# Kernel tuning notes

Measured on AMD Instinct MI355X. Metric: run time of the kernel, lower is better.

## Reference

```python
import jax, jax.numpy as jnp
import numpy as np

V, E, U, B, S = 32000, 512, 1024, 16, 128
BN_EPS = 1e-3  # keras BatchNormalization default


def setup_inputs() -> dict:
    key = jax.random.key(0)
    ks = jax.random.split(key, 12)
    w = 0.05  # small init keeps the relu-activated LSTM recurrence stable
    return {
        "inputs": jax.random.randint(ks[0], (B, S), 0, V),
        "enc_hidden": jax.random.normal(ks[1], (B, U), jnp.float32) * 0.1,
        "enc_cell": jax.random.normal(ks[2], (B, U), jnp.float32) * 0.1,
        "emb": jax.random.normal(ks[3], (V, E), jnp.float32) * w,
        "Wx": jax.random.normal(ks[4], (E, 4 * U), jnp.float32) * w,
        "Wh": jax.random.normal(ks[5], (U, 4 * U), jnp.float32) * w,
        "b": jnp.zeros((4 * U,), jnp.float32),
        "gamma": jnp.ones((U,), jnp.float32),
        "beta": jnp.zeros((U,), jnp.float32),
        "mov_mean": jnp.zeros((U,), jnp.float32),
        "mov_var": jnp.ones((U,), jnp.float32),
        "W1": jax.random.normal(ks[6], (U, U), jnp.float32) * w,
        "b1": jnp.zeros((U,), jnp.float32),
        "W2": jax.random.normal(ks[7], (U, V), jnp.float32) * w,
        "b2": jnp.zeros((V,), jnp.float32),
    }


def _lstm_relu(xg, mask, h0, c0, Wh):
    # xg: [S,B,4U] precomputed input gates; mask: [S,B] (mask_zero semantics)
    def step(carry, inp):
        h, c = carry
        g, m = inp
        z = g + h @ Wh  # [B,4U]
        i, f, cc, o = jnp.split(z, 4, axis=-1)  # keras gate order i,f,c,o
        i = jax.nn.sigmoid(i)
        f = jax.nn.sigmoid(f)
        o = jax.nn.sigmoid(o)
        cc = jax.nn.relu(cc)  # activation='relu' on candidate
        c_new = f * c + i * cc
        h_new = o * jax.nn.relu(c_new)  # activation='relu' on output
        m = m[:, None]
        h_new = jnp.where(m, h_new, h)  # masked step: carry state/output
        c_new = jnp.where(m, c_new, c)
        return (h_new, c_new), h_new

    (_, _), hs = jax.lax.scan(step, (h0, c0), (xg, mask))
    return hs  # [S,B,U]


def reference(inputs, enc_hidden, enc_cell, emb, Wx, Wh, b, gamma, beta,
              mov_mean, mov_var, W1, b1, W2, b2):
    x = emb[inputs]                       # [B,S,E]
    mask = (inputs != 0)                  # mask_zero=True
    xg = jnp.einsum("bse,eg->bsg", x, Wx) + b   # [B,S,4U]
    hs = _lstm_relu(xg.transpose(1, 0, 2), mask.T, enc_hidden, enc_cell, Wh)
    h = hs.transpose(1, 0, 2)             # [B,S,U]
    # BatchNorm (inference: moving statistics), Dropout is identity at inference
    hbn = (h - mov_mean) * jax.lax.rsqrt(mov_var + BN_EPS) * gamma + beta
    d1 = jax.nn.relu(hbn @ W1 + b1)       # [B,S,U]
    logits = d1 @ W2 + b2                 # [B,S,V]
    return jax.nn.softmax(logits, axis=-1)
```

## Files before the change

### kernel.cpp

```cpp
#include <hip/hip_runtime.h>
#include <hip/hip_bf16.h>
#include <stdint.h>

typedef unsigned short u16;
typedef unsigned int u32;
typedef unsigned long long u64;
typedef __attribute__((ext_vector_type(4))) float f32x4;
typedef __attribute__((ext_vector_type(8))) short s16x8;

#define AT_LD(p)    __hip_atomic_load((p), __ATOMIC_RELAXED, __HIP_MEMORY_SCOPE_AGENT)
#define AT_ST(p, v) __hip_atomic_store((p), (v), __ATOMIC_RELAXED, __HIP_MEMORY_SCOPE_AGENT)


static __device__ __forceinline__ u16 f2bf(float f) {
  union { float f; unsigned u; } v; v.f = f;
  unsigned r = v.u + 0x7FFFu + ((v.u >> 16) & 1u);
  return (u16)(r >> 16);
}

static __device__ __forceinline__ void gload_lds16(const void* g, void* l) {
  __builtin_amdgcn_global_load_lds(
      (const __attribute__((address_space(1))) unsigned int*)(uintptr_t)g,
      (__attribute__((address_space(3))) unsigned int*)(uintptr_t)l,
      16, 0, 0);
}

static __device__ __forceinline__ int swzB(int B) {
  int pos = (B >> 4) & 127;
  int row = (B >> 11) & 15;
  int slot = (pos ^ row ^ (pos >> 3)) & 7;
  int npos = (pos & 0x78) | slot;
  return (B & ~0x7F0) | (npos << 4);
}


__global__ void embed_kernel(const int* __restrict__ inputs,
                             const float* __restrict__ emb,
                             u16* __restrict__ xbf) {
  int i = blockIdx.x * 256 + threadIdx.x;
  int row = i >> 6;
  int e0 = (i & 63) << 3;
  int tok = inputs[row];
  const float* src = emb + (size_t)tok * 512 + e0;
  s16x8 o;
#pragma unroll
  for (int j = 0; j < 8; ++j) o[j] = (short)f2bf(src[j]);
  *(s16x8*)(xbf + (size_t)row * 512 + e0) = o;
}

__global__ void mask_kernel(const int* __restrict__ inputs, u64* __restrict__ mb) {
  int t = threadIdx.x;
  if (t < 32) {
    int b = t >> 1, h = t & 1;
    u64 m = 0;
    for (int j = 0; j < 64; ++j)
      m |= (u64)(inputs[b * 128 + h * 64 + j] != 0) << j;
    mb[t] = m;
  }
}

__global__ void transpose_bf16(const float* __restrict__ W, u16* __restrict__ Wt,
                               int K, int N) {
  __shared__ float t[32][33];
  int ntn = N >> 5;
  int tn = blockIdx.x % ntn, tk = blockIdx.x / ntn;
  int n0 = tn << 5, k0 = tk << 5;
  int tx = threadIdx.x & 31, ty = threadIdx.x >> 5;
#pragma unroll
  for (int j = 0; j < 4; ++j) {
    int k = ty * 4 + j;
    t[k][tx] = W[(size_t)(k0 + k) * N + n0 + tx];
  }
  __syncthreads();
#pragma unroll
  for (int j = 0; j < 4; ++j) {
    int n = ty * 4 + j;
    Wt[(size_t)(n0 + n) * K + k0 + tx] = f2bf(t[tx][n]);
  }
}

template <int MODE>
__global__ __launch_bounds__(256)
void gemm_bf16(const u16* __restrict__ A, const u16* __restrict__ Bt,
               const float* __restrict__ bias, void* __restrict__ Cptr,
               float* __restrict__ rowsum, int M, int N, int K) {
  (void)M;
  __shared__ u16 sA[128 * 32];
  __shared__ u16 sB[128 * 32];
  const int nbn = N >> 7;
  const int nwg = gridDim.x;
  int bid = blockIdx.x;
  int q = nwg >> 3;
  int swz = (bid & 7) * q + (bid >> 3);
  int bm = swz / nbn, bn = swz % nbn;
  const int brow = bm << 7, bcol = bn << 7;

  const int tid = threadIdx.x;
  const int lane = tid & 63;
  const int wv = tid >> 6;
  const int wr = (wv >> 1) * 64, wc = (wv & 1) * 64;
  const int ln = lane & 15, kh = lane >> 4;

  const int srow = tid >> 2;
  const int kch = (tid & 3) << 3;

  f32x4 acc[4][4] = {};

  const int nk = K >> 5;
  const u16* Abase = A + (size_t)(brow + srow) * K + kch;
  const u16* Bbase = Bt + (size_t)(bcol + srow) * K + kch;
  const size_t rstride = (size_t)64 * K;
  u16* lA = sA + srow * 32 + kch;
  u16* lB = sB + srow * 32 + kch;

  for (int kt = 0; kt < nk; ++kt) {
    const int k0 = kt << 5;
    gload_lds16(Abase + k0, lA);
    gload_lds16(Abase + rstride + k0, lA + 64 * 32);
    gload_lds16(Bbase + k0, lB);
    gload_lds16(Bbase + rstride + k0, lB + 64 * 32);
    __syncthreads();
    s16x8 aF[4], bF[4];
#pragma unroll
    for (int m = 0; m < 4; ++m)
      aF[m] = *(const s16x8*)(sA + (wr + m * 16 + ln) * 32 + kh * 8);
#pragma unroll
    for (int n = 0; n < 4; ++n)
      bF[n] = *(const s16x8*)(sB + (wc + n * 16 + ln) * 32 + kh * 8);
#pragma unroll
    for (int m = 0; m < 4; ++m)
#pragma unroll
      for (int n = 0; n < 4; ++n)
        acc[m][n] = __builtin_amdgcn_mfma_f32_16x16x32_bf16(aF[m], bF[n], acc[m][n], 0, 0, 0);
    __syncthreads();
  }

  const int browq = brow + wr;
  const int bcolq = bcol + wc;

  if (MODE == 1) {
    u16* O = (u16*)Cptr;
#pragma unroll
    for (int n = 0; n < 4; ++n) {
      int gcol = bcolq + n * 16 + ln;
      float bv = bias[gcol];
#pragma unroll
      for (int m = 0; m < 4; ++m)
#pragma unroll
        for (int r = 0; r < 4; ++r) {
          int grow = browq + m * 16 + kh * 4 + r;
          float v = fmaxf(acc[m][n][r] + bv, 0.f);
          O[(size_t)grow * N + gcol] = f2bf(v);
        }
    }
  } else {
    float* O = (float*)Cptr;
    float rs[4][4] = {};
#pragma unroll
    for (int n = 0; n < 4; ++n) {
      int gcol = bcolq + n * 16 + ln;
      float bv = bias[gcol];
#pragma unroll
      for (int m = 0; m < 4; ++m)
#pragma unroll
        for (int r = 0; r < 4; ++r) {
          int grow = browq + m * 16 + kh * 4 + r;
          float v = acc[m][n][r] + bv;
          if (MODE == 2) { v = __expf(v); rs[m][r] += v; }
          O[(size_t)grow * N + gcol] = v;
        }
    }
    if (MODE == 2) {
#pragma unroll
      for (int m = 0; m < 4; ++m)
#pragma unroll
        for (int r = 0; r < 4; ++r) {
          float v = rs[m][r];
          v += __shfl_xor(v, 1);
          v += __shfl_xor(v, 2);
          v += __shfl_xor(v, 4);
          v += __shfl_xor(v, 8);
          if (ln == 0) atomicAdd(&rowsum[browq + m * 16 + kh * 4 + r], v);
        }
    }
  }
}

__global__ __launch_bounds__(256, 1)
void lstm_kernel(const float* __restrict__ xg,
                 const u16* __restrict__ Wht,
                 const u64* __restrict__ maskb,
                 const float* __restrict__ ench, const float* __restrict__ encc,
                 const float* __restrict__ gamma, const float* __restrict__ beta,
                 const float* __restrict__ mmean, const float* __restrict__ mvar,
                 u32* __restrict__ hbuf32,
                 u16* __restrict__ hbn,
                 u32* __restrict__ cnt) {
  __shared__ char hA[32 * 1024];

  const int wg = blockIdx.x;
  const int u0 = wg << 4;
  const int tid = threadIdx.x;
  const int lane = tid & 63;
  const int wv = tid >> 6;
  const int ln = lane & 15, kh = lane >> 4;

  const int g = ln & 3;
  const int ul = ln >> 2;
  const int unit = u0 + wv * 4 + ul;

  s16x8 bW[32];
  {
    const u16* wrow = Wht + (size_t)(g * 1024 + unit) * 1024 + kh * 8;
#pragma unroll
    for (int kt = 0; kt < 32; ++kt)
      bW[kt] = *(const s16x8*)(wrow + kt * 32);
  }

  float cellR[4], holdR[4];
  u64 mA[4], mB[4];
  const float bn_s = gamma[unit] * rsqrtf(mvar[unit] + 1e-3f);
  const float bn_b = beta[unit] - mmean[unit] * bn_s;
#pragma unroll
  for (int r = 0; r < 4; ++r) {
    int batch = kh * 4 + r;
    cellR[r] = encc[batch * 1024 + unit];
    holdR[r] = ench[batch * 1024 + unit];
    mA[r] = maskb[batch * 2];
    mB[r] = maskb[batch * 2 + 1];
  }

#pragma unroll
  for (int r = 0; r < 4; ++r) {
    u32 w = (u32)f2bf(holdR[r]);
    u32 pw = (u32)__shfl_xor((int)w, 4);
    if ((ln & 7) == 0) {
      int batch = kh * 4 + r;
      int B = batch * 2048 + unit * 2;
      AT_ST((u32*)((char*)hbuf32 + B), (w & 0xFFFFu) | (pw << 16));
    }
  }
  asm volatile("s_waitcnt vmcnt(0)" ::: "memory");
  __syncthreads();
  if (tid == 0) {
    (void)__hip_atomic_fetch_add(cnt, 1, __ATOMIC_RELAXED, __HIP_MEMORY_SCOPE_AGENT);
    int c = 0;
    while (AT_LD((const u32*)cnt) < 64u) { if (++c > (1 << 20)) break; }
  }
  __syncthreads();

  const size_t bstride = (size_t)128 * 4096;
  const float* xbase = xg + (size_t)(kh * 4) * bstride + g * 1024 + unit;
  float xgr[4];
#pragma unroll
  for (int r = 0; r < 4; ++r) xgr[r] = xbase[r * bstride];

  for (int s = 0; s < 128; ++s) {
    const u64* src = (const u64*)((const char*)hbuf32 + (s & 1) * 32768) + tid;
    u64 st[16];
#pragma unroll
    for (int k = 0; k < 16; ++k) st[k] = AT_LD(src + k * 256);
#pragma unroll
    for (int k = 0; k < 16; ++k)
      *(u64*)(hA + swzB(k * 2048 + tid * 8)) = st[k];
    __syncthreads();

    f32x4 acc0 = {0.f, 0.f, 0.f, 0.f};
    f32x4 acc1 = {0.f, 0.f, 0.f, 0.f};
#pragma unroll
    for (int kt = 0; kt < 32; kt += 2) {
      s16x8 a0 = *(const s16x8*)(hA + swzB(ln * 2048 + kt * 64 + kh * 16));
      acc0 = __builtin_amdgcn_mfma_f32_16x16x32_bf16(a0, bW[kt], acc0, 0, 0, 0);
      s16x8 a1 = *(const s16x8*)(hA + swzB(ln * 2048 + (kt + 1) * 64 + kh * 16));
      acc1 = __builtin_amdgcn_mfma_f32_16x16x32_bf16(a1, bW[kt + 1], acc1, 0, 0, 0);
    }

    u16 hbb[4], hbnb[4];
#pragma unroll
    for (int r = 0; r < 4; ++r) {
      float z = acc0[r] + acc1[r] + xgr[r];
      float sig = 1.f / (1.f + __expf(-z));
      float val = (g == 2) ? fmaxf(z, 0.f) : sig;
      float v1 = __shfl_xor(val, 1);
      float v2 = __shfl_xor(val, 2);
      float v3 = __shfl_xor(val, 3);
      float cnew = v1 * cellR[r] + val * v2;
      float hnew = v3 * fmaxf(cnew, 0.f);
      u64 mm = (s < 64) ? mA[r] : mB[r];
      if (!((mm >> (s & 63)) & 1)) { cnew = cellR[r]; hnew = holdR[r]; }
      cellR[r] = cnew;
      holdR[r] = hnew;
      hbb[r] = f2bf(hnew);
      hbnb[r] = f2bf(hnew * bn_s + bn_b);
    }

#pragma unroll
    for (int r = 0; r < 4; ++r) {
      u32 w = (u32)hbb[r] | ((u32)hbnb[r] << 16);
      u32 pw = (u32)__shfl_xor((int)w, 4);
      if ((ln & 7) == 0) {
        int batch = kh * 4 + r;
        u32 hpair = (w & 0xFFFFu) | ((pw & 0xFFFFu) << 16);
        u32 bnpair = (w >> 16) | (pw & 0xFFFF0000u);
        if (s < 127) {
          int B = batch * 2048 + unit * 2;
          AT_ST((u32*)((char*)hbuf32 + ((s + 1) & 1) * 32768 + B), hpair);
        }
        *(u32*)((char*)hbn + (size_t)(batch * 128 + s) * 2048 + unit * 2) = bnpair;
      }
    }

    if (s < 127) {
      asm volatile("s_waitcnt vmcnt(0)" ::: "memory");
      __syncthreads();
      if (tid == 0)
        (void)__hip_atomic_fetch_add(cnt, 1, __ATOMIC_RELAXED, __HIP_MEMORY_SCOPE_AGENT);
      {
        const float* xb = xbase + (size_t)(s + 1) * 4096;
#pragma unroll
        for (int r = 0; r < 4; ++r) xgr[r] = xb[r * bstride];
      }
      if (tid == 0) {
        const u32 target = (u32)(s + 2) * 64u;
        int c = 0;
        while (AT_LD((const u32*)cnt) < target) { if (++c > (1 << 20)) break; }
      }
      __syncthreads();
    }
  }
}


__global__ void rcp_kernel(float* rs) {
  int i = blockIdx.x * 256 + threadIdx.x;
  rs[i] = 1.0f / rs[i];
}

__global__ void scale_kernel(float* __restrict__ out, const float* __restrict__ rinv) {
  const int total4 = 16384000;
  for (int i = blockIdx.x * 256 + threadIdx.x; i < total4; i += gridDim.x * 256) {
    float4* p = (float4*)out + i;
    float4 v = *p;
    int row = i / 8000;
    float sF = rinv[row];
    v.x *= sF; v.y *= sF; v.z *= sF; v.w *= sF;
    *p = v;
  }
}


extern "C" void kernel_launch(void* const* d_in, const int* in_sizes, int n_in,
                              void* d_out, int out_size, void* d_ws, size_t ws_size,
                              hipStream_t stream) {
  (void)in_sizes; (void)n_in; (void)out_size;
  const int*   inputs = (const int*)d_in[0];
  const float* ench   = (const float*)d_in[1];
  const float* encc   = (const float*)d_in[2];
  const float* emb    = (const float*)d_in[3];
  const float* Wx     = (const float*)d_in[4];
  const float* Wh     = (const float*)d_in[5];
  const float* bb     = (const float*)d_in[6];
  const float* gamma  = (const float*)d_in[7];
  const float* beta   = (const float*)d_in[8];
  const float* mmean  = (const float*)d_in[9];
  const float* mvar   = (const float*)d_in[10];
  const float* W1     = (const float*)d_in[11];
  const float* b1     = (const float*)d_in[12];
  const float* W2     = (const float*)d_in[13];
  const float* b2     = (const float*)d_in[14];
  float* out = (float*)d_out;

  char* p = (char*)d_ws;
  u32*   cnt    = (u32*)(p + 0);
  float* rowsum = (float*)(p + 1024);
  u64*   maskb  = (u64*)(p + 10240);
  u32*   hbuf32 = (u32*)(p + 16384);
  size_t off = 81920;
  u16*   xbf  = (u16*)(p + off);     off += (size_t)2048 * 512 * 2;
  u16*   Wxt  = (u16*)(p + off);     off += (size_t)4096 * 512 * 2;
  u16*   Wht  = (u16*)(p + off);     off += (size_t)4096 * 1024 * 2;
  u16*   W1t  = (u16*)(p + off);     off += (size_t)1024 * 1024 * 2;
  u16*   W2t  = (u16*)(p + off);     off += (size_t)32000 * 1024 * 2;
  float* xg   = (float*)(p + off);   off += (size_t)2048 * 4096 * 4;
  u16*   hbn  = (u16*)(p + off);     off += (size_t)2048 * 1024 * 2;
  u16*   d1   = (u16*)(p + off);     off += (size_t)2048 * 1024 * 2;
  if (ws_size < off) return;

  hipMemsetAsync(d_ws, 0, 9216, stream);

  embed_kernel<<<512, 256, 0, stream>>>(inputs, emb, xbf);
  mask_kernel<<<1, 64, 0, stream>>>(inputs, maskb);
  transpose_bf16<<<(512 / 32) * (4096 / 32), 256, 0, stream>>>(Wx, Wxt, 512, 4096);
  transpose_bf16<<<(1024 / 32) * (4096 / 32), 256, 0, stream>>>(Wh, Wht, 1024, 4096);
  transpose_bf16<<<(1024 / 32) * (1024 / 32), 256, 0, stream>>>(W1, W1t, 1024, 1024);
  transpose_bf16<<<(1024 / 32) * (32000 / 32), 256, 0, stream>>>(W2, W2t, 1024, 32000);

  gemm_bf16<0><<<16 * 32, 256, 0, stream>>>(xbf, Wxt, bb, xg, nullptr, 2048, 4096, 512);

  lstm_kernel<<<64, 256, 0, stream>>>(xg, Wht, maskb, ench, encc, gamma, beta,
                                      mmean, mvar, hbuf32, hbn, cnt);

  gemm_bf16<1><<<16 * 8, 256, 0, stream>>>(hbn, W1t, b1, d1, nullptr, 2048, 1024, 1024);
  gemm_bf16<2><<<16 * 250, 256, 0, stream>>>(d1, W2t, b2, out, rowsum, 2048, 32000, 1024);

  rcp_kernel<<<8, 256, 0, stream>>>(rowsum);
  scale_kernel<<<2048, 256, 0, stream>>>(out, rowsum);
}
```

Measured before the change: 1.049 ms.

## Split LSTM recurrent K-reduction across two wave groups with LDS partial-sum combine

```diff
diff --git a/kernel.cpp b/kernel.cpp
--- a/kernel.cpp
+++ b/kernel.cpp
@@ -186,7 +186,7 @@
   }
 }
 
-__global__ __launch_bounds__(256, 1)
+__global__ __launch_bounds__(512, 1)
 void lstm_kernel(const float* __restrict__ xg,
                  const u16* __restrict__ Wht,
                  const u64* __restrict__ maskb,
@@ -197,133 +197,154 @@
                  u16* __restrict__ hbn,
                  u32* __restrict__ cnt) {
   __shared__ char hA[32 * 1024];
+  __shared__ float zxP[8][16][16];
 
   const int wg = blockIdx.x;
   const int u0 = wg << 4;
   const int tid = threadIdx.x;
   const int lane = tid & 63;
   const int wv = tid >> 6;
-  const int ln = lane & 15, kh = lane >> 4;
+  const int ln = lane & 15, khq = lane >> 4;
+  const int cg = wv & 3, kh2 = wv >> 2;
 
   const int g = ln & 3;
-  const int ul = ln >> 2;
-  const int unit = u0 + wv * 4 + ul;
-
-  s16x8 bW[32];
+  const int unit = u0 + cg * 4 + (ln >> 2);
+
+  s16x8 bW[16];
   {
-    const u16* wrow = Wht + (size_t)(g * 1024 + unit) * 1024 + kh * 8;
-#pragma unroll
-    for (int kt = 0; kt < 32; ++kt)
+    const u16* wrow = Wht + (size_t)(g * 1024 + unit) * 1024 + kh2 * 512 + khq * 8;
+#pragma unroll
+    for (int kt = 0; kt < 16; ++kt)
       bW[kt] = *(const s16x8*)(wrow + kt * 32);
-  }
-
-  float cellR[4], holdR[4];
-  u64 mA[4], mB[4];
-  const float bn_s = gamma[unit] * rsqrtf(mvar[unit] + 1e-3f);
-  const float bn_b = beta[unit] - mmean[unit] * bn_s;
-#pragma unroll
-  for (int r = 0; r < 4; ++r) {
-    int batch = kh * 4 + r;
-    cellR[r] = encc[batch * 1024 + unit];
-    holdR[r] = ench[batch * 1024 + unit];
-    mA[r] = maskb[batch * 2];
-    mB[r] = maskb[batch * 2 + 1];
-  }
-
-#pragma unroll
-  for (int r = 0; r < 4; ++r) {
-    u32 w = (u32)f2bf(holdR[r]);
-    u32 pw = (u32)__shfl_xor((int)w, 4);
-    if ((ln & 7) == 0) {
-      int batch = kh * 4 + r;
-      int B = batch * 2048 + unit * 2;
-      AT_ST((u32*)((char*)hbuf32 + B), (w & 0xFFFFu) | (pw << 16));
-    }
+#pragma unroll
+    for (int kt = 0; kt < 16; ++kt)
+      asm volatile("" : "+v"(bW[kt]));
+  }
+
+  float cellR[4] = {}, holdR[4] = {}, xgr[4] = {};
+  u64 mA[4] = {}, mB[4] = {};
+  float bn_s = 0.f, bn_b = 0.f;
+  const size_t bstride = (size_t)128 * 4096;
+  const float* xbase = xg + (size_t)(khq * 4) * bstride + g * 1024 + unit;
+  if (kh2 == 0) {
+    bn_s = gamma[unit] * rsqrtf(mvar[unit] + 1e-3f);
+    bn_b = beta[unit] - mmean[unit] * bn_s;
+#pragma unroll
+    for (int r = 0; r < 4; ++r) {
+      int batch = khq * 4 + r;
+      cellR[r] = encc[batch * 1024 + unit];
+      holdR[r] = ench[batch * 1024 + unit];
+      mA[r] = maskb[batch * 2];
+      mB[r] = maskb[batch * 2 + 1];
+    }
+#pragma unroll
+    for (int r = 0; r < 4; ++r) {
+      u32 w = (u32)f2bf(holdR[r]);
+      u32 pw = (u32)__shfl_xor((int)w, 4);
+      if ((ln & 7) == 0) {
+        int batch = khq * 4 + r;
+        AT_ST((u32*)((char*)hbuf32 + batch * 2048 + unit * 2), (w & 0xFFFFu) | (pw << 16));
+      }
+    }
+#pragma unroll
+    for (int r = 0; r < 4; ++r) xgr[r] = xbase[r * bstride];
   }
   asm volatile("s_waitcnt vmcnt(0)" ::: "memory");
   __syncthreads();
   if (tid == 0) {
-    (void)__hip_atomic_fetch_add(cnt, 1, __ATOMIC_RELAXED, __HIP_MEMORY_SCOPE_AGENT);
-    int c = 0;
-    while (AT_LD((const u32*)cnt) < 64u) { if (++c > (1 << 20)) break; }
+    int oldv = (int)__hip_atomic_fetch_add(cnt, 1, __ATOMIC_RELAXED, __HIP_MEMORY_SCOPE_AGENT);
+    if (oldv != 63) {
+      int c = 0;
+      while (AT_LD((const u32*)cnt) < 64u) { if (++c > (1 << 20)) break; }
+    }
   }
   __syncthreads();
 
-  const size_t bstride = (size_t)128 * 4096;
-  const float* xbase = xg + (size_t)(kh * 4) * bstride + g * 1024 + unit;
-  float xgr[4];
-#pragma unroll
-  for (int r = 0; r < 4; ++r) xgr[r] = xbase[r * bstride];
-
   for (int s = 0; s < 128; ++s) {
-    const u64* src = (const u64*)((const char*)hbuf32 + (s & 1) * 32768) + tid;
-    u64 st[16];
-#pragma unroll
-    for (int k = 0; k < 16; ++k) st[k] = AT_LD(src + k * 256);
-#pragma unroll
-    for (int k = 0; k < 16; ++k)
-      *(u64*)(hA + swzB(k * 2048 + tid * 8)) = st[k];
+    u64 st[8];
+    {
+      const u64* base = (const u64*)((const char*)hbuf32 + (s & 1) * 32768) + tid;
+#pragma unroll
+      for (int k = 0; k < 8; ++k) {
+        const u64* pp = base + k * 512;
+        asm volatile("global_load_dwordx2 %0, %1, off sc0 sc1" : "=v"(st[k]) : "v"(pp));
+      }
+      asm volatile("s_waitcnt vmcnt(0)" ::: "memory");
+      __builtin_amdgcn_sched_barrier(0);
+#pragma unroll
+      for (int k = 0; k < 8; ++k)
+        *(u64*)(hA + swzB((tid + k * 512) * 8)) = st[k];
+    }
     __syncthreads();
 
     f32x4 acc0 = {0.f, 0.f, 0.f, 0.f};
     f32x4 acc1 = {0.f, 0.f, 0.f, 0.f};
 #pragma unroll
-    for (int kt = 0; kt < 32; kt += 2) {
-      s16x8 a0 = *(const s16x8*)(hA + swzB(ln * 2048 + kt * 64 + kh * 16));
+    for (int kt = 0; kt < 16; kt += 2) {
+      s16x8 a0 = *(const s16x8*)(hA + swzB(ln * 2048 + kh2 * 1024 + kt * 64 + khq * 16));
       acc0 = __builtin_amdgcn_mfma_f32_16x16x32_bf16(a0, bW[kt], acc0, 0, 0, 0);
-      s16x8 a1 = *(const s16x8*)(hA + swzB(ln * 2048 + (kt + 1) * 64 + kh * 16));
+      s16x8 a1 = *(const s16x8*)(hA + swzB(ln * 2048 + kh2 * 1024 + (kt + 1) * 64 + khq * 16));
       acc1 = __builtin_amdgcn_mfma_f32_16x16x32_bf16(a1, bW[kt + 1], acc1, 0, 0, 0);
     }
-
-    u16 hbb[4], hbnb[4];
-#pragma unroll
-    for (int r = 0; r < 4; ++r) {
-      float z = acc0[r] + acc1[r] + xgr[r];
-      float sig = 1.f / (1.f + __expf(-z));
-      float val = (g == 2) ? fmaxf(z, 0.f) : sig;
-      float v1 = __shfl_xor(val, 1);
-      float v2 = __shfl_xor(val, 2);
-      float v3 = __shfl_xor(val, 3);
-      float cnew = v1 * cellR[r] + val * v2;
-      float hnew = v3 * fmaxf(cnew, 0.f);
-      u64 mm = (s < 64) ? mA[r] : mB[r];
-      if (!((mm >> (s & 63)) & 1)) { cnew = cellR[r]; hnew = holdR[r]; }
-      cellR[r] = cnew;
-      holdR[r] = hnew;
-      hbb[r] = f2bf(hnew);
-      hbnb[r] = f2bf(hnew * bn_s + bn_b);
-    }
-
-#pragma unroll
-    for (int r = 0; r < 4; ++r) {
-      u32 w = (u32)hbb[r] | ((u32)hbnb[r] << 16);
-      u32 pw = (u32)__shfl_xor((int)w, 4);
-      if ((ln & 7) == 0) {
-        int batch = kh * 4 + r;
-        u32 hpair = (w & 0xFFFFu) | ((pw & 0xFFFFu) << 16);
-        u32 bnpair = (w >> 16) | (pw & 0xFFFF0000u);
-        if (s < 127) {
-          int B = batch * 2048 + unit * 2;
-          AT_ST((u32*)((char*)hbuf32 + ((s + 1) & 1) * 32768 + B), hpair);
+    f32x4 accs = acc0 + acc1;
+#pragma unroll
+    for (int r = 0; r < 4; ++r) zxP[wv][khq * 4 + r][ln] = accs[r];
+    __syncthreads();
+
+    if (kh2 == 0) {
+      u16 hbb[4], hbnb[4];
+#pragma unroll
+      for (int r = 0; r < 4; ++r) {
+        int batch = khq * 4 + r;
+        float z = zxP[cg][batch][ln] + zxP[cg + 4][batch][ln] + xgr[r];
+        float sig = 1.f / (1.f + __expf(-z));
+        float val = (g == 2) ? fmaxf(z, 0.f) : sig;
+        float v1 = __shfl_xor(val, 1);
+        float v2 = __shfl_xor(val, 2);
+        float v3 = __shfl_xor(val, 3);
+        float cnew = v1 * cellR[r] + val * v2;
+        float hnew = v3 * fmaxf(cnew, 0.f);
+        u64 mm = (s < 64) ? mA[r] : mB[r];
+        if (!((mm >> (s & 63)) & 1)) { cnew = cellR[r]; hnew = holdR[r]; }
+        cellR[r] = cnew;
+        holdR[r] = hnew;
+        hbb[r] = f2bf(hnew);
+        hbnb[r] = f2bf(hnew * bn_s + bn_b);
+      }
+#pragma unroll
+      for (int r = 0; r < 4; ++r) {
+        u32 w = (u32)hbb[r] | ((u32)hbnb[r] << 16);
+        u32 pw = (u32)__shfl_xor((int)w, 4);
+        if ((ln & 7) == 0) {
+          int batch = khq * 4 + r;
+          u32 hpair = (w & 0xFFFFu) | ((pw & 0xFFFFu) << 16);
+          u32 bnpair = (w >> 16) | (pw & 0xFFFF0000u);
+          if (s < 127) {
+            int B = batch * 2048 + unit * 2;
+            AT_ST((u32*)((char*)hbuf32 + ((s + 1) & 1) * 32768 + B), hpair);
+          }
+          *(u32*)((char*)hbn + (size_t)(batch * 128 + s) * 2048 + unit * 2) = bnpair;
         }
-        *(u32*)((char*)hbn + (size_t)(batch * 128 + s) * 2048 + unit * 2) = bnpair;
       }
     }
 
     if (s < 127) {
       asm volatile("s_waitcnt vmcnt(0)" ::: "memory");
       __syncthreads();
+      int oldv = -1;
       if (tid == 0)
-        (void)__hip_atomic_fetch_add(cnt, 1, __ATOMIC_RELAXED, __HIP_MEMORY_SCOPE_AGENT);
-      {
+        oldv = (int)__hip_atomic_fetch_add(cnt, 1, __ATOMIC_RELAXED, __HIP_MEMORY_SCOPE_AGENT);
+      if (kh2 == 0) {
         const float* xb = xbase + (size_t)(s + 1) * 4096;
 #pragma unroll
         for (int r = 0; r < 4; ++r) xgr[r] = xb[r * bstride];
       }
       if (tid == 0) {
         const u32 target = (u32)(s + 2) * 64u;
-        int c = 0;
-        while (AT_LD((const u32*)cnt) < target) { if (++c > (1 << 20)) break; }
+        if (oldv != (int)target - 1) {
+          int c = 0;
+          while (AT_LD((const u32*)cnt) < target) { if (++c > (1 << 20)) break; }
+        }
       }
       __syncthreads();
     }
@@ -397,7 +418,7 @@
 
   gemm_bf16<0><<<16 * 32, 256, 0, stream>>>(xbf, Wxt, bb, xg, nullptr, 2048, 4096, 512);
 
-  lstm_kernel<<<64, 256, 0, stream>>>(xg, Wht, maskb, ench, encc, gamma, beta,
+  lstm_kernel<<<64, 512, 0, stream>>>(xg, Wht, maskb, ench, encc, gamma, beta,
                                       mmean, mvar, hbuf32, hbn, cnt);
 
   gemm_bf16<1><<<16 * 8, 256, 0, stream>>>(hbn, W1t, b1, d1, nullptr, 2048, 1024, 1024);
```

After: 1.003 ms. 4.4% less time.
